# Kernel tuning notes

Measured on AMD Instinct MI355X. Metric: run time of the kernel, lower is better.

The kernel has to match this reference:

```python
import jax, jax.numpy as jnp
import numpy as np

N_HEAD = 16
N_KV_HEAD = 4
HEAD_DIM = 64
VE_CH = 12  # min(12, n_embd)


def apply_rotary_emb(x, cos, sin):
    d = x.shape[3] // 2
    x1, x2 = x[..., :d], x[..., d:]
    return jnp.concatenate([x1 * cos + x2 * sin, x1 * -sin + x2 * cos], axis=3)


def rms_norm(x):
    return x * jax.lax.rsqrt(jnp.mean(jnp.square(x), axis=-1, keepdims=True) + 1e-6)


def setup_inputs() -> dict:
    key = jax.random.key(0)
    ks = jax.random.split(key, 9)
    B, T, C = 2, 2048, 1024
    s = 0.02
    return {
        "x": jax.random.normal(ks[0], (B, T, C), jnp.float32),
        "ve": jax.random.normal(ks[1], (B, T, N_KV_HEAD * HEAD_DIM), jnp.float32),
        "cos": jax.random.normal(ks[2], (1, T, 1, HEAD_DIM // 2), jnp.float32),
        "sin": jax.random.normal(ks[3], (1, T, 1, HEAD_DIM // 2), jnp.float32),
        "Wq": jax.random.normal(ks[4], (C, C), jnp.float32) * s,
        "Wk": jax.random.normal(ks[5], (N_KV_HEAD * HEAD_DIM, C), jnp.float32) * s,
        "Wv": jax.random.normal(ks[6], (N_KV_HEAD * HEAD_DIM, C), jnp.float32) * s,
        "Wo": jax.random.normal(ks[7], (C, C), jnp.float32) * s,
        "Wg": jax.random.normal(ks[8], (N_KV_HEAD, VE_CH), jnp.float32) * s,
    }


def reference(x, ve, cos, sin, Wq, Wk, Wv, Wo, Wg):
    B, T, C = x.shape
    q = (x @ Wq.T).reshape(B, T, N_HEAD, HEAD_DIM)
    k = (x @ Wk.T).reshape(B, T, N_KV_HEAD, HEAD_DIM)
    v = (x @ Wv.T).reshape(B, T, N_KV_HEAD, HEAD_DIM)

    # value-embedding gate
    ve_r = ve.reshape(B, T, N_KV_HEAD, HEAD_DIM)
    gate = 3.0 * jax.nn.sigmoid(x[..., :VE_CH] @ Wg.T)  # [B,T,n_kv_head]
    v = v + gate[..., None] * ve_r

    q = apply_rotary_emb(q, cos, sin)
    k = apply_rotary_emb(k, cos, sin)
    q = rms_norm(q) * 1.2
    k = rms_norm(k) * 1.2

    # GQA: expand kv heads
    r = N_HEAD // N_KV_HEAD
    k = jnp.repeat(k, r, axis=2)
    v = jnp.repeat(v, r, axis=2)

    # [B,H,T,D]
    q = q.transpose(0, 2, 1, 3)
    k = k.transpose(0, 2, 1, 3)
    v = v.transpose(0, 2, 1, 3)

    scale = 1.0 / np.sqrt(HEAD_DIM).astype(np.float32)
    scores = jnp.einsum("bhqd,bhkd->bhqk", q, k) * scale
    causal = jnp.tril(jnp.ones((T, T), dtype=bool))
    scores = jnp.where(causal, scores, jnp.float32(-jnp.inf))
    att = jax.nn.softmax(scores, axis=-1)
    y = jnp.einsum("bhqk,bhkd->bhqd", att, v)
    y = y.transpose(0, 2, 1, 3).reshape(B, T, C)
    return y @ Wo.T
```

## Files before the change

### kernel.cpp

```cpp
#include <hip/hip_runtime.h>
#include <stdint.h>

#define B_SZ 2
#define T_SZ 2048
#define C_SZ 1024
#define NH   16
#define NKV  4
#define HD   64
#define KVD  256
#define QKV_N 1536

typedef __attribute__((ext_vector_type(8))) short bf16x8;
typedef __attribute__((ext_vector_type(4))) float f32x4;

#define GL(p) ((const __attribute__((address_space(1))) void*)(p))
#define LD(p) ((__attribute__((address_space(3))) void*)(p))

__device__ inline unsigned short f2bf(float f) {
  union { float f; unsigned u; } v; v.f = f;
  unsigned u = v.u;
  unsigned r = (u + 0x7fffu + ((u >> 16) & 1u)) >> 16;
  return (unsigned short)r;
}
__device__ inline unsigned short bftrunc(float f) {
  union { float f; unsigned u; } v; v.f = f;
  return (unsigned short)(v.u >> 16);
}

struct CvtArgs {
  const float *s0, *s1, *s2, *s3, *s4;
  unsigned short *d0, *d1, *d2, *d3, *d4;
  const float *x, *Wg;
  float *gate;
};
__global__ __launch_bounds__(256) void cvt_all(CvtArgs a) {
  int blk = blockIdx.x, tid = threadIdx.x;
  if (blk >= 6656) {
    int idx = (blk - 6656) * 256 + tid;
    int bt = idx >> 2, kh = idx & 3;
    float s = 0.f;
#pragma unroll
    for (int j = 0; j < 12; j++) s += a.x[(size_t)bt * C_SZ + j] * a.Wg[kh * 12 + j];
    a.gate[idx] = 3.f / (1.f + __expf(-s));
    return;
  }
  const float* s; unsigned short* d; int i;
  if      (blk < 4096) { s = a.s0; d = a.d0; i = blk * 256 + tid; }
  else if (blk < 5120) { s = a.s1; d = a.d1; i = (blk - 4096) * 256 + tid; }
  else if (blk < 5376) { s = a.s2; d = a.d2; i = (blk - 5120) * 256 + tid; }
  else if (blk < 5632) { s = a.s3; d = a.d3; i = (blk - 5376) * 256 + tid; }
  else                 { s = a.s4; d = a.d4; i = (blk - 5632) * 256 + tid; }
  float4 f = ((const float4*)s)[i];
  ushort4 o;
  o.x = f2bf(f.x); o.y = f2bf(f.y); o.z = f2bf(f.z); o.w = f2bf(f.w);
  ((ushort4*)d)[i] = o;
}

#define GEMM_PROLOG(A, Bm, K)                                                        \
  __shared__ unsigned short As[2][64 * 64];                                          \
  __shared__ unsigned short Bs[2][128 * 64];                                         \
  int tid  = threadIdx.x;                                                            \
  int lane = tid & 63;                                                               \
  int wave = tid >> 6;                                                               \
  int quad = lane >> 4;                                                              \
  int l16  = lane & 15;                                                              \
  int m0 = blockIdx.y * 64;                                                          \
  int n0 = blockIdx.x * 128;                                                         \
  int wm = (wave & 1) * 32;                                                          \
  int wn = (wave >> 1) * 64;                                                         \
  f32x4 acc[2][4];                                                                   \
  _Pragma("unroll") for (int i = 0; i < 2; i++)                                      \
    _Pragma("unroll") for (int j = 0; j < 4; j++)                                    \
      acc[i][j] = (f32x4){0.f, 0.f, 0.f, 0.f};                                       \
  int lrow = lane >> 3;                                 \
  int lcol = ((lane & 7) ^ lrow) * 8;                 \
  int sA = wave * 16;                                                                \
  int sB = wave * 32;                                                                \
  const unsigned short* aP0 = &A[(size_t)(m0 + sA + lrow) * K + lcol];               \
  const unsigned short* aP1 = aP0 + 8 * (size_t)K;                                   \
  const unsigned short* bP0 = &Bm[(size_t)(n0 + sB + lrow) * K + lcol];              \
  const unsigned short* bP1 = bP0 + 8 * (size_t)K;                                   \
  const unsigned short* bP2 = bP0 + 16 * (size_t)K;                                  \
  const unsigned short* bP3 = bP0 + 24 * (size_t)K;                                  \
  __builtin_amdgcn_global_load_lds(GL(aP0), LD(&As[0][(sA     ) * 64]), 16, 0, 0);   \
  __builtin_amdgcn_global_load_lds(GL(aP1), LD(&As[0][(sA +  8) * 64]), 16, 0, 0);   \
  __builtin_amdgcn_global_load_lds(GL(bP0), LD(&Bs[0][(sB     ) * 64]), 16, 0, 0);   \
  __builtin_amdgcn_global_load_lds(GL(bP1), LD(&Bs[0][(sB +  8) * 64]), 16, 0, 0);   \
  __builtin_amdgcn_global_load_lds(GL(bP2), LD(&Bs[0][(sB + 16) * 64]), 16, 0, 0);   \
  __builtin_amdgcn_global_load_lds(GL(bP3), LD(&Bs[0][(sB + 24) * 64]), 16, 0, 0);   \
  int swz = l16 & 7;                                                                 \
  int nk = K >> 6;                                                                   \
  for (int ki = 0; ki < nk; ki++) {                                                  \
    int cur = ki & 1, nxt = cur ^ 1;                                                 \
    __syncthreads();                                                                 \
    if (ki + 1 < nk) {                                                               \
      int k0 = (ki + 1) << 6;                                                        \
      __builtin_amdgcn_global_load_lds(GL(aP0 + k0), LD(&As[nxt][(sA     ) * 64]), 16, 0, 0); \
      __builtin_amdgcn_global_load_lds(GL(aP1 + k0), LD(&As[nxt][(sA +  8) * 64]), 16, 0, 0); \
      __builtin_amdgcn_global_load_lds(GL(bP0 + k0), LD(&Bs[nxt][(sB     ) * 64]), 16, 0, 0); \
      __builtin_amdgcn_global_load_lds(GL(bP1 + k0), LD(&Bs[nxt][(sB +  8) * 64]), 16, 0, 0); \
      __builtin_amdgcn_global_load_lds(GL(bP2 + k0), LD(&Bs[nxt][(sB + 16) * 64]), 16, 0, 0); \
      __builtin_amdgcn_global_load_lds(GL(bP3 + k0), LD(&Bs[nxt][(sB + 24) * 64]), 16, 0, 0); \
    }                                                                                \
    _Pragma("unroll") for (int p = 0; p < 2; p++) {                                  \
      bf16x8 af[2], bfr[4];                                                          \
      _Pragma("unroll") for (int i = 0; i < 2; i++)                                  \
        af[i] = *(const bf16x8*)&As[cur][(wm + i * 16 + l16) * 64 + (((p * 4 + quad) ^ swz) * 8)]; \
      _Pragma("unroll") for (int j = 0; j < 4; j++)                                  \
        bfr[j] = *(const bf16x8*)&Bs[cur][(wn + j * 16 + l16) * 64 + (((p * 4 + quad) ^ swz) * 8)]; \
      _Pragma("unroll") for (int i = 0; i < 2; i++)                                  \
        _Pragma("unroll") for (int j = 0; j < 4; j++)                                \
          acc[i][j] = __builtin_amdgcn_mfma_f32_16x16x32_bf16(af[i], bfr[j], acc[i][j], 0, 0, 0); \
    }                                                                                \
  }

__global__ __launch_bounds__(256) void gemm_bt(const unsigned short* __restrict__ A,
                                               const unsigned short* __restrict__ Bm,
                                               float* __restrict__ C,
                                               int N, int K) {
  GEMM_PROLOG(A, Bm, K)
#pragma unroll
  for (int i = 0; i < 2; i++) {
#pragma unroll
    for (int j = 0; j < 4; j++) {
      int col = n0 + wn + j * 16 + l16;
#pragma unroll
      for (int r = 0; r < 4; r++) {
        int row = m0 + wm + i * 16 + quad * 4 + r;
        C[(size_t)row * N + col] = acc[i][j][r];
      }
    }
  }
}

__global__ __launch_bounds__(256) void gemm_qkv(const unsigned short* __restrict__ A,
                                                const unsigned short* __restrict__ Bm,
                                                const float* __restrict__ ve,
                                                const float* __restrict__ cosb,
                                                const float* __restrict__ sinb,
                                                const float* __restrict__ gateArr,
                                                unsigned short* __restrict__ qa,
                                                unsigned short* __restrict__ ka,
                                                unsigned short* __restrict__ vtmp) {
  const int K = C_SZ;
  GEMM_PROLOG(A, Bm, K)

  int colbase = n0 + wn;
  if (colbase < 1280) {
    int isQ = colbase < 1024;
    int h   = isQ ? (colbase >> 6) : ((colbase - 1024) >> 6);
    float scale = isQ ? (0.15f * 1.44269504088896f) : 1.2f;
    unsigned short* dst = isQ ? qa : ka;
    int nheads = isQ ? NH : NKV;
#pragma unroll
    for (int i = 0; i < 2; i++) {
#pragma unroll
      for (int r = 0; r < 4; r++) {
        int row = m0 + wm + i * 16 + quad * 4 + r;
        int t = row & (T_SZ - 1), b = row >> 11;
        float a10 = acc[i][0][r], a11 = acc[i][1][r];
        float a20 = acc[i][2][r], a21 = acc[i][3][r];
        float cv0 = cosb[t * 32 + l16],      sv0 = sinb[t * 32 + l16];
        float cv1 = cosb[t * 32 + 16 + l16], sv1 = sinb[t * 32 + 16 + l16];
        float o10 =  a10 * cv0 + a20 * sv0;
        float o11 =  a11 * cv1 + a21 * sv1;
        float o20 = -a10 * sv0 + a20 * cv0;
        float o21 = -a11 * sv1 + a21 * cv1;
        float ssq = o10 * o10 + o11 * o11 + o20 * o20 + o21 * o21;
        ssq += __shfl_xor(ssq, 1);
        ssq += __shfl_xor(ssq, 2);
        ssq += __shfl_xor(ssq, 4);
        ssq += __shfl_xor(ssq, 8);
        float rn = rsqrtf(ssq * (1.f / 64.f) + 1e-6f) * scale;
        size_t base = ((size_t)(b * nheads + h) * T_SZ + t) * HD;
        dst[base + l16]      = f2bf(o10 * rn);
        dst[base + 16 + l16] = f2bf(o11 * rn);
        dst[base + 32 + l16] = f2bf(o20 * rn);
        dst[base + 48 + l16] = f2bf(o21 * rn);
      }
    }
  } else {
    int kh = (colbase - 1280) >> 6;
#pragma unroll
    for (int i = 0; i < 2; i++) {
#pragma unroll
      for (int r = 0; r < 4; r++) {
        int row = m0 + wm + i * 16 + quad * 4 + r;
        float g = gateArr[row * 4 + kh];
#pragma unroll
        for (int j = 0; j < 4; j++) {
          int d = j * 16 + l16;
          float val = acc[i][j][r] + g * ve[(size_t)row * KVD + kh * HD + d];
          vtmp[(size_t)row * KVD + kh * HD + d] = f2bf(val);
        }
      }
    }
  }
}

__global__ __launch_bounds__(256) void v_transpose(const unsigned short* __restrict__ vtmp,
                                                   unsigned short* __restrict__ vt) {
  __shared__ unsigned short tile[64 * 68];
  int blk = blockIdx.x;
  int tb = blk & 31, kh = (blk >> 5) & 3, b = blk >> 7;
  int tid = threadIdx.x;
  int r = tid >> 2, c = (tid & 3) * 16;
  const unsigned short* src = &vtmp[((size_t)(b * T_SZ + tb * 64 + r)) * KVD + kh * HD + c];
  uint4 x0 = *(const uint4*)(src);
  uint4 x1 = *(const uint4*)(src + 8);
  *(uint2*)&tile[r * 68 + c]      = *(uint2*)&x0;
  *(uint2*)&tile[r * 68 + c + 4]  = *((uint2*)&x0 + 1);
  *(uint2*)&tile[r * 68 + c + 8]  = *(uint2*)&x1;
  *(uint2*)&tile[r * 68 + c + 12] = *((uint2*)&x1 + 1);
  __syncthreads();
  int d = tid >> 2, tc = (tid & 3) * 16;
  ushort4 o0, o1, o2, o3;
  o0.x = tile[(tc + 0) * 68 + d];  o0.y = tile[(tc + 1) * 68 + d];
  o0.z = tile[(tc + 2) * 68 + d];  o0.w = tile[(tc + 3) * 68 + d];
  o1.x = tile[(tc + 4) * 68 + d];  o1.y = tile[(tc + 5) * 68 + d];
  o1.z = tile[(tc + 6) * 68 + d];  o1.w = tile[(tc + 7) * 68 + d];
  o2.x = tile[(tc + 8) * 68 + d];  o2.y = tile[(tc + 9) * 68 + d];
  o2.z = tile[(tc + 10) * 68 + d]; o2.w = tile[(tc + 11) * 68 + d];
  o3.x = tile[(tc + 12) * 68 + d]; o3.y = tile[(tc + 13) * 68 + d];
  o3.z = tile[(tc + 14) * 68 + d]; o3.w = tile[(tc + 15) * 68 + d];
  unsigned short* dst = &vt[((size_t)(b * NKV + kh) * HD + d) * T_SZ + tb * 64 + tc];
  *(ushort4*)(dst)      = o0;
  *(ushort4*)(dst + 4)  = o1;
  *(ushort4*)(dst + 8)  = o2;
  *(ushort4*)(dst + 12) = o3;
}

#define KST 72
#define PST 72
__global__ __launch_bounds__(256) void attn(const unsigned short* __restrict__ qa,
                                            const unsigned short* __restrict__ ka,
                                            const unsigned short* __restrict__ vt,
                                            unsigned short* __restrict__ y) {
  int bid = blockIdx.x;
  int half = bid >> 8, r = bid & 255;
  int qt = half ? (r & 15) : 15 - (r & 15);
  int bh = (half << 4) | (r >> 4);
  int b = bh >> 4, h = bh & 15;
  int kh = h >> 2;
  int tid = threadIdx.x;
  int wave = tid >> 6, lane = tid & 63;
  int quad = lane >> 4, l16 = lane & 15;

  __shared__ unsigned short Ks[2][64 * KST];
  __shared__ unsigned short Vs[2][64 * KST];
  __shared__ unsigned short Ps[128 * PST];
  unsigned short* Pw = &Ps[(wave * 32) * PST];

  bf16x8 bq[2][2];
#pragma unroll
  for (int qi = 0; qi < 2; qi++) {
    int tq = qt * 128 + wave * 32 + qi * 16 + l16;
    const unsigned short* qp = &qa[((size_t)(b * NH + h) * T_SZ + tq) * HD];
    bq[qi][0] = *(const bf16x8*)&qp[quad * 8];
    bq[qi][1] = *(const bf16x8*)&qp[32 + quad * 8];
  }

  const unsigned short one_bf = 0x3F80;
  bf16x8 vones = {(short)one_bf, (short)one_bf, (short)one_bf, (short)one_bf,
                  (short)one_bf, (short)one_bf, (short)one_bf, (short)one_bf};

  f32x4 oacc[2][4];
  f32x4 lacc[2];
#pragma unroll
  for (int qi = 0; qi < 2; qi++) {
    lacc[qi] = (f32x4){0.f, 0.f, 0.f, 0.f};
#pragma unroll
    for (int d = 0; d < 4; d++) oacc[qi][d] = (f32x4){0.f, 0.f, 0.f, 0.f};
  }

  int lr = tid >> 2;
  int lc = (tid & 3) * 16;

  const unsigned short* kbase = &ka[(size_t)(b * NKV + kh) * T_SZ * HD];
  const unsigned short* vbase = &vt[(size_t)(b * NKV + kh) * HD * T_SZ];

  int nj = 2 * qt + 2;

  {
    const unsigned short* kp = &kbase[(size_t)lr * HD + lc];
    const unsigned short* vp = &vbase[(size_t)lr * T_SZ + lc];
    uint4 k0 = *(const uint4*)(kp);
    uint4 k1 = *(const uint4*)(kp + 8);
    uint4 v0 = *(const uint4*)(vp);
    uint4 v1 = *(const uint4*)(vp + 8);
    *(uint4*)&Ks[0][lr * KST + lc]     = k0;
    *(uint4*)&Ks[0][lr * KST + lc + 8] = k1;
    *(uint4*)&Vs[0][lr * KST + lc]     = v0;
    *(uint4*)&Vs[0][lr * KST + lc + 8] = v1;
  }

  int qrow0 = qt * 128 + wave * 32;

  for (int j = 0; j < nj; j++) {
    int cur = j & 1, nxt = cur ^ 1;
    __syncthreads();

    uint4 k0, k1, v0, v1;
    bool pf = (j + 1 < nj);
    if (pf) {
      const unsigned short* kp = &kbase[(size_t)((j + 1) * 64 + lr) * HD + lc];
      const unsigned short* vp = &vbase[(size_t)lr * T_SZ + (j + 1) * 64 + lc];
      k0 = *(const uint4*)(kp);
      k1 = *(const uint4*)(kp + 8);
      v0 = *(const uint4*)(vp);
      v1 = *(const uint4*)(vp + 8);
    }

    f32x4 st[4][2];
#pragma unroll
    for (int tb = 0; tb < 4; tb++) {
      bf16x8 ak0 = *(const bf16x8*)&Ks[cur][(tb * 16 + l16) * KST + quad * 8];
      bf16x8 ak1 = *(const bf16x8*)&Ks[cur][(tb * 16 + l16) * KST + 32 + quad * 8];
#pragma unroll
      for (int qi = 0; qi < 2; qi++) {
        f32x4 s = (f32x4){0.f, 0.f, 0.f, 0.f};
        s = __builtin_amdgcn_mfma_f32_16x16x32_bf16(ak0, bq[qi][0], s, 0, 0, 0);
        s = __builtin_amdgcn_mfma_f32_16x16x32_bf16(ak1, bq[qi][1], s, 0, 0, 0);
        st[tb][qi] = s;
      }
    }

#pragma unroll
    for (int qi = 0; qi < 2; qi++) {
      int qlow = qrow0 + qi * 16;
      if (j * 64 + 63 > qlow) {
        int qg = qlow + l16;
#pragma unroll
        for (int tb = 0; tb < 4; tb++) {
          int tg = j * 64 + tb * 16 + quad * 4;
#pragma unroll
          for (int i = 0; i < 4; i++) {
            if (tg + i > qg) st[tb][qi][i] = -__builtin_inff();
          }
        }
      }
#pragma unroll
      for (int tb = 0; tb < 4; tb++) {
        ushort4 w;
        w.x = bftrunc(__builtin_amdgcn_exp2f(st[tb][qi][0]));
        w.y = bftrunc(__builtin_amdgcn_exp2f(st[tb][qi][1]));
        w.z = bftrunc(__builtin_amdgcn_exp2f(st[tb][qi][2]));
        w.w = bftrunc(__builtin_amdgcn_exp2f(st[tb][qi][3]));
        *(ushort4*)&Pw[(qi * 16 + l16) * PST + tb * 16 + quad * 4] = w;
      }
    }

    bf16x8 ap[2][2];
#pragma unroll
    for (int qi = 0; qi < 2; qi++) {
      ap[qi][0] = *(const bf16x8*)&Pw[(qi * 16 + l16) * PST + quad * 8];
      ap[qi][1] = *(const bf16x8*)&Pw[(qi * 16 + l16) * PST + 32 + quad * 8];
      lacc[qi] = __builtin_amdgcn_mfma_f32_16x16x32_bf16(ap[qi][0], vones, lacc[qi], 0, 0, 0);
      lacc[qi] = __builtin_amdgcn_mfma_f32_16x16x32_bf16(ap[qi][1], vones, lacc[qi], 0, 0, 0);
    }
#pragma unroll
    for (int d = 0; d < 4; d++) {
      bf16x8 bv0 = *(const bf16x8*)&Vs[cur][(d * 16 + l16) * KST + quad * 8];
      bf16x8 bv1 = *(const bf16x8*)&Vs[cur][(d * 16 + l16) * KST + 32 + quad * 8];
#pragma unroll
      for (int qi = 0; qi < 2; qi++) {
        oacc[qi][d] = __builtin_amdgcn_mfma_f32_16x16x32_bf16(ap[qi][0], bv0, oacc[qi][d], 0, 0, 0);
        oacc[qi][d] = __builtin_amdgcn_mfma_f32_16x16x32_bf16(ap[qi][1], bv1, oacc[qi][d], 0, 0, 0);
      }
    }

    if (pf) {
      *(uint4*)&Ks[nxt][lr * KST + lc]     = k0;
      *(uint4*)&Ks[nxt][lr * KST + lc + 8] = k1;
      *(uint4*)&Vs[nxt][lr * KST + lc]     = v0;
      *(uint4*)&Vs[nxt][lr * KST + lc + 8] = v1;
    }
  }

#pragma unroll
  for (int qi = 0; qi < 2; qi++) {
#pragma unroll
    for (int i = 0; i < 4; i++) {
      int tq = qrow0 + qi * 16 + quad * 4 + i;
      float inv = 1.f / lacc[qi][i];
#pragma unroll
      for (int d = 0; d < 4; d++) {
        y[((size_t)(b * T_SZ) + tq) * C_SZ + h * HD + d * 16 + l16] = f2bf(oacc[qi][d][i] * inv);
      }
    }
  }
}

extern "C" void kernel_launch(void* const* d_in, const int* in_sizes, int n_in,
                              void* d_out, int out_size, void* d_ws, size_t ws_size,
                              hipStream_t stream) {
  const float* x    = (const float*)d_in[0];
  const float* ve   = (const float*)d_in[1];
  const float* cosb = (const float*)d_in[2];
  const float* sinb = (const float*)d_in[3];
  const float* Wq   = (const float*)d_in[4];
  const float* Wk   = (const float*)d_in[5];
  const float* Wv   = (const float*)d_in[6];
  const float* Wo   = (const float*)d_in[7];
  const float* Wg   = (const float*)d_in[8];
  float* out = (float*)d_out;

  const size_t MB = 1024 * 1024;
  char* ws = (char*)d_ws;
  unsigned short* xb    = (unsigned short*)(ws);
  unsigned short* wqkvb = (unsigned short*)(ws + 8 * MB);
  unsigned short* wob   = (unsigned short*)(ws + 11 * MB);
  unsigned short* qab   = (unsigned short*)(ws + 13 * MB);
  unsigned short* kab   = (unsigned short*)(ws + 21 * MB);
  unsigned short* vtb   = (unsigned short*)(ws + 23 * MB);
  float*          gateA = (float*)(ws + 25 * MB);
  unsigned short* vtmp  = (unsigned short*)(ws + 26 * MB);
  unsigned short* yb    = xb;

  CvtArgs ca;
  ca.s0 = x;  ca.d0 = xb;
  ca.s1 = Wq; ca.d1 = wqkvb;
  ca.s2 = Wk; ca.d2 = wqkvb + 1024 * 1024;
  ca.s3 = Wv; ca.d3 = wqkvb + 1280 * 1024;
  ca.s4 = Wo; ca.d4 = wob;
  ca.x = x; ca.Wg = Wg; ca.gate = gateA;
  cvt_all<<<6720, 256, 0, stream>>>(ca);

  gemm_qkv<<<dim3(QKV_N / 128, (B_SZ * T_SZ) / 64), 256, 0, stream>>>(
      xb, wqkvb, ve, cosb, sinb, gateA, qab, kab, vtmp);

  v_transpose<<<256, 256, 0, stream>>>(vtmp, vtb);

  attn<<<512, 256, 0, stream>>>(qab, kab, vtb, yb);

  gemm_bt<<<dim3(C_SZ / 128, (B_SZ * T_SZ) / 64), 256, 0, stream>>>(
      yb, wob, out, C_SZ, C_SZ);
}
```

Baseline: 170.1 us.

## Load K/V tiles directly into LDS with XOR-swizzled layout in attention

Replaces register-staged K/V tile prefetch (global load to VGPRs, then LDS store after compute) with direct global-to-LDS loads, and replaces padded row stride with an XOR swizzle on 8-element chunks to avoid bank conflicts. This is meant to cut VGPR pressure and the separate LDS write pass, and to shrink LDS footprint. It relies on the single barrier per iteration plus the hardware's wait behaviour to make the async LDS writes visible, which is a synchronisation risk.

```diff
diff --git a/kernel.cpp b/kernel.cpp
--- a/kernel.cpp
+++ b/kernel.cpp
@@ -230,7 +230,6 @@
   *(ushort4*)(dst + 12) = o3;
 }
 
-#define KST 72
 #define PST 72
 __global__ __launch_bounds__(256) void attn(const unsigned short* __restrict__ qa,
                                             const unsigned short* __restrict__ ka,
@@ -246,8 +245,8 @@
   int wave = tid >> 6, lane = tid & 63;
   int quad = lane >> 4, l16 = lane & 15;
 
-  __shared__ unsigned short Ks[2][64 * KST];
-  __shared__ unsigned short Vs[2][64 * KST];
+  __shared__ unsigned short Ks[2][64 * 64];
+  __shared__ unsigned short Vs[2][64 * 64];
   __shared__ unsigned short Ps[128 * PST];
   unsigned short* Pw = &Ps[(wave * 32) * PST];
 
@@ -273,49 +272,46 @@
     for (int d = 0; d < 4; d++) oacc[qi][d] = (f32x4){0.f, 0.f, 0.f, 0.f};
   }
 
-  int lr = tid >> 2;
-  int lc = (tid & 3) * 16;
-
+  int row8 = lane >> 3;
+  int slot = lane & 7;
+  int scol = (slot ^ row8) * 8;
   const unsigned short* kbase = &ka[(size_t)(b * NKV + kh) * T_SZ * HD];
   const unsigned short* vbase = &vt[(size_t)(b * NKV + kh) * HD * T_SZ];
+  const unsigned short* kp0 = &kbase[(size_t)(wave * 16 + row8) * HD + scol];
+  const unsigned short* kp1 = kp0 + 8 * HD;
+  const unsigned short* vp0 = &vbase[(size_t)(wave * 16 + row8) * T_SZ + scol];
+  const unsigned short* vp1 = vp0 + 8 * T_SZ;
+  unsigned short* dK0 = &Ks[0][(wave * 16) * 64];
+  unsigned short* dV0 = &Vs[0][(wave * 16) * 64];
 
   int nj = 2 * qt + 2;
 
-  {
-    const unsigned short* kp = &kbase[(size_t)lr * HD + lc];
-    const unsigned short* vp = &vbase[(size_t)lr * T_SZ + lc];
-    uint4 k0 = *(const uint4*)(kp);
-    uint4 k1 = *(const uint4*)(kp + 8);
-    uint4 v0 = *(const uint4*)(vp);
-    uint4 v1 = *(const uint4*)(vp + 8);
-    *(uint4*)&Ks[0][lr * KST + lc]     = k0;
-    *(uint4*)&Ks[0][lr * KST + lc + 8] = k1;
-    *(uint4*)&Vs[0][lr * KST + lc]     = v0;
-    *(uint4*)&Vs[0][lr * KST + lc + 8] = v1;
-  }
+  __builtin_amdgcn_global_load_lds(GL(kp0), LD(&Ks[0][(wave * 16) * 64]), 16, 0, 0);
+  __builtin_amdgcn_global_load_lds(GL(kp1), LD(&Ks[0][(wave * 16 + 8) * 64]), 16, 0, 0);
+  __builtin_amdgcn_global_load_lds(GL(vp0), LD(&Vs[0][(wave * 16) * 64]), 16, 0, 0);
+  __builtin_amdgcn_global_load_lds(GL(vp1), LD(&Vs[0][(wave * 16 + 8) * 64]), 16, 0, 0);
 
   int qrow0 = qt * 128 + wave * 32;
+  int swz = l16 & 7;
 
   for (int j = 0; j < nj; j++) {
     int cur = j & 1, nxt = cur ^ 1;
     __syncthreads();
 
-    uint4 k0, k1, v0, v1;
-    bool pf = (j + 1 < nj);
-    if (pf) {
-      const unsigned short* kp = &kbase[(size_t)((j + 1) * 64 + lr) * HD + lc];
-      const unsigned short* vp = &vbase[(size_t)lr * T_SZ + (j + 1) * 64 + lc];
-      k0 = *(const uint4*)(kp);
-      k1 = *(const uint4*)(kp + 8);
-      v0 = *(const uint4*)(vp);
-      v1 = *(const uint4*)(vp + 8);
+    if (j + 1 < nj) {
+      size_t ko = (size_t)(j + 1) * 64 * HD;
+      int    vo = (j + 1) * 64;
+      __builtin_amdgcn_global_load_lds(GL(kp0 + ko), LD(&Ks[nxt][(wave * 16) * 64]), 16, 0, 0);
+      __builtin_amdgcn_global_load_lds(GL(kp1 + ko), LD(&Ks[nxt][(wave * 16 + 8) * 64]), 16, 0, 0);
+      __builtin_amdgcn_global_load_lds(GL(vp0 + vo), LD(&Vs[nxt][(wave * 16) * 64]), 16, 0, 0);
+      __builtin_amdgcn_global_load_lds(GL(vp1 + vo), LD(&Vs[nxt][(wave * 16 + 8) * 64]), 16, 0, 0);
     }
 
     f32x4 st[4][2];
 #pragma unroll
     for (int tb = 0; tb < 4; tb++) {
-      bf16x8 ak0 = *(const bf16x8*)&Ks[cur][(tb * 16 + l16) * KST + quad * 8];
-      bf16x8 ak1 = *(const bf16x8*)&Ks[cur][(tb * 16 + l16) * KST + 32 + quad * 8];
+      bf16x8 ak0 = *(const bf16x8*)&Ks[cur][(tb * 16 + l16) * 64 + ((quad ^ swz) * 8)];
+      bf16x8 ak1 = *(const bf16x8*)&Ks[cur][(tb * 16 + l16) * 64 + (((quad + 4) ^ swz) * 8)];
 #pragma unroll
       for (int qi = 0; qi < 2; qi++) {
         f32x4 s = (f32x4){0.f, 0.f, 0.f, 0.f};
@@ -360,21 +356,14 @@
     }
 #pragma unroll
     for (int d = 0; d < 4; d++) {
-      bf16x8 bv0 = *(const bf16x8*)&Vs[cur][(d * 16 + l16) * KST + quad * 8];
-      bf16x8 bv1 = *(const bf16x8*)&Vs[cur][(d * 16 + l16) * KST + 32 + quad * 8];
+      bf16x8 bv0 = *(const bf16x8*)&Vs[cur][(d * 16 + l16) * 64 + ((quad ^ swz) * 8)];
+      bf16x8 bv1 = *(const bf16x8*)&Vs[cur][(d * 16 + l16) * 64 + (((quad + 4) ^ swz) * 8)];
 #pragma unroll
       for (int qi = 0; qi < 2; qi++) {
         oacc[qi][d] = __builtin_amdgcn_mfma_f32_16x16x32_bf16(ap[qi][0], bv0, oacc[qi][d], 0, 0, 0);
         oacc[qi][d] = __builtin_amdgcn_mfma_f32_16x16x32_bf16(ap[qi][1], bv1, oacc[qi][d], 0, 0, 0);
       }
     }
-
-    if (pf) {
-      *(uint4*)&Ks[nxt][lr * KST + lc]     = k0;
-      *(uint4*)&Ks[nxt][lr * KST + lc + 8] = k1;
-      *(uint4*)&Vs[nxt][lr * KST + lc]     = v0;
-      *(uint4*)&Vs[nxt][lr * KST + lc + 8] = v1;
-    }
   }
 
 #pragma unroll
@@ -389,6 +378,7 @@
       }
     }
   }
+  (void)dK0; (void)dV0;
 }
 
 extern "C" void kernel_launch(void* const* d_in, const int* in_sizes, int n_in,
```

New measurement: 179.6 us. +5.6%, slower.
